# Optimization experiments

Hardware: AMD Instinct MI355X
Metric: run time of the kernel (lower is better)

Reference implementation:

```python
import jax, jax.numpy as jnp
import numpy as np

F, LP, NL, DG = 65536, 8, 8192, 64
D = 32  # path_state_dim == link_state_dim
ITERS = 8
MS = {'flow_traffic': (0.5, 2.0), 'flow_length': (0.5, 2.0), 'flow_loss_packet': (0.1, 5.0),
      'flow_propag_delay': (0.2, 3.0), 'link_capacity': (1.0, 1.0)}


def gru_cell(h, x, w, u, b):
    # Keras GRUCell (reset_after=True); gate order z, r, h
    mx = x @ w + b[0]
    mh = h @ u + b[1]
    xz, xr, xh = jnp.split(mx, 3, axis=-1)
    hz, hr, hh = jnp.split(mh, 3, axis=-1)
    z = jax.nn.sigmoid(xz + hz)
    r = jax.nn.sigmoid(xr + hr)
    c = jnp.tanh(xh + r * hh)
    return z * h + (1.0 - z) * c


def setup_inputs() -> dict:
    key = jax.random.key(0)
    ks = jax.random.split(key, 24)
    g = lambda i, shape: jax.random.normal(ks[i], shape, jnp.float32) * 0.1
    return dict(
        flow_traffic=jax.random.uniform(ks[0], (F, 1), jnp.float32),
        flow_length=jax.random.uniform(ks[1], (F, 1), jnp.float32),
        flow_loss_packet=jax.random.uniform(ks[2], (F, 1), jnp.float32),
        flow_propag_delay=jax.random.uniform(ks[3], (F, 1), jnp.float32),
        flow_packet_size=jax.random.uniform(ks[4], (F, 1), jnp.float32),
        link_capacity=jax.random.uniform(ks[5], (NL, 1), jnp.float32) + 0.5,
        link_to_flow=jax.random.randint(ks[6], (F, LP), 0, NL),
        flow_to_link_flow=jax.random.randint(ks[7], (NL, DG), 0, F),
        flow_to_link_pos=jax.random.randint(ks[8], (NL, DG), 0, LP + 1),
        fe_w1=g(9, (4, D)), fe_b1=jnp.zeros(D), fe_w2=g(10, (D, D)), fe_b2=jnp.zeros(D),
        le_w1=g(11, (2, D)), le_b1=jnp.zeros(D), le_w2=g(12, (D, D)), le_b2=jnp.zeros(D),
        att_w=g(13, (D, D)), att_b=jnp.zeros(D),
        pg_w=g(14, (D, 3 * D)), pg_u=g(15, (D, 3 * D)), pg_b=jnp.zeros((2, 3 * D)),
        lg_w=g(16, (D, 3 * D)), lg_u=g(17, (D, 3 * D)), lg_b=jnp.zeros((2, 3 * D)),
        ro_w1=g(18, (D, D // 2)), ro_b1=jnp.zeros(D // 2),
        ro_w2=g(19, (D // 2, D // 4)), ro_b2=jnp.zeros(D // 4),
        ro_w3=g(20, (D // 4, 1)), ro_b3=jnp.zeros(1),
    )


def reference(flow_traffic, flow_length, flow_loss_packet, flow_propag_delay, flow_packet_size,
              link_capacity, link_to_flow, flow_to_link_flow, flow_to_link_pos,
              fe_w1, fe_b1, fe_w2, fe_b2, le_w1, le_b1, le_w2, le_b2, att_w, att_b,
              pg_w, pg_u, pg_b, lg_w, lg_u, lg_b, ro_w1, ro_b1, ro_w2, ro_b2, ro_w3, ro_b3):
    norm = lambda x, k: (x - MS[k][0]) * MS[k][1]
    # per-link load: mean of traffic of flows crossing it / capacity  -> [NL,1]
    load = jnp.mean(flow_traffic[flow_to_link_flow], axis=1) / link_capacity
    pf = jnp.concatenate([norm(flow_traffic, 'flow_traffic'), norm(flow_length, 'flow_length'),
                          norm(flow_loss_packet, 'flow_loss_packet'),
                          norm(flow_propag_delay, 'flow_propag_delay')], axis=1)
    path_state = jax.nn.selu(jax.nn.selu(pf @ fe_w1 + fe_b1) @ fe_w2 + fe_b2)  # [F,D]
    lf = jnp.concatenate([norm(link_capacity, 'link_capacity'), load], axis=1)
    link_state = jax.nn.selu(jax.nn.selu(lf @ le_w1 + le_b1) @ le_w2 + le_b2)  # [NL,D]

    pss = None
    for _ in range(ITERS):
        link_gather = link_state[link_to_flow]  # [F,LP,D]
        prev = path_state

        def step(h, x):
            h2 = gru_cell(h, x, pg_w, pg_u, pg_b)
            return h2, h2

        path_state, seq = jax.lax.scan(step, prev, jnp.swapaxes(link_gather, 0, 1))
        seq = jnp.swapaxes(seq, 0, 1)  # [F,LP,D]
        pss = jnp.concatenate([prev[:, None, :], seq], axis=1)  # [F,LP+1,D]
        path_gather = pss[flow_to_link_flow, flow_to_link_pos]  # [NL,DG,D]
        attn = jax.nn.leaky_relu(path_gather @ att_w + att_b, negative_slope=0.2)
        score = jax.nn.softmax(attn, axis=-1)  # K.softmax default axis=-1
        agg = jnp.sum(score * path_gather, axis=1)  # [NL,D]
        link_state = gru_cell(link_state, agg, lg_w, lg_u, lg_b)

    h = jax.nn.selu(pss[:, 1:] @ ro_w1 + ro_b1)
    h = jax.nn.selu(h @ ro_w2 + ro_b2)
    occupancy = jax.nn.softplus(h @ ro_w3 + ro_b3)  # [F,LP,1]
    capacity_gather = link_capacity[link_to_flow]  # [F,LP,1]
    delay = jnp.sum(occupancy / capacity_gather, axis=1)  # [F,1]
    return delay + flow_propag_delay
```

## Files before the change

kernel.cpp:

```cpp
#include <hip/hip_runtime.h>
#include <hip/hip_bf16.h>
#include <cstddef>

#define F_    65536
#define LP_   8
#define NL_   8192
#define DG_   64
#define D_    32
#define ITERS_ 8

typedef short bf16x8 __attribute__((ext_vector_type(8)));
typedef float f32x2 __attribute__((ext_vector_type(2)));
typedef float f32x4 __attribute__((ext_vector_type(4)));
typedef float f32x16 __attribute__((ext_vector_type(16)));
typedef unsigned int u32x4 __attribute__((ext_vector_type(4)));


__device__ __forceinline__ float sigmoidf_(float x) { return 1.0f / (1.0f + __expf(-x)); }
__device__ __forceinline__ float tanhf_(float x)    { return 1.0f - 2.0f / (__expf(2.0f * x) + 1.0f); }
__device__ __forceinline__ float seluf_(float x) {
    const float a = 1.6732632423543772f, s = 1.0507009873554805f;
    return x > 0.0f ? s * x : s * a * (__expf(x) - 1.0f);
}
__device__ __forceinline__ float softplusf_(float x) { return x > 20.0f ? x : log1pf(__expf(x)); }

#define REP32(M) M(0)M(1)M(2)M(3)M(4)M(5)M(6)M(7)M(8)M(9)M(10)M(11)M(12)M(13)M(14)M(15) \
                 M(16)M(17)M(18)M(19)M(20)M(21)M(22)M(23)M(24)M(25)M(26)M(27)M(28)M(29)M(30)M(31)

#define BC32(src, i) __int_as_float(__builtin_amdgcn_ds_swizzle(__float_as_int(src), ((i) << 5)))

__device__ __forceinline__ unsigned int cvtpk_bf16(float a, float b) {
    unsigned int r;
    asm("v_cvt_pk_bf16_f32 %0, %1, %2" : "=v"(r) : "v"(a), "v"(b));
    return r;
}
__device__ __forceinline__ float bf_lo(unsigned int u) { return __uint_as_float(u << 16); }
__device__ __forceinline__ float bf_hi(unsigned int u) { return __uint_as_float(u & 0xFFFF0000u); }

__device__ __forceinline__ void mk_frag_w(f32x4 v0, f32x4 v1, u32x4& uh, u32x4& ul) {
    uh.x = cvtpk_bf16(v0.x, v0.y);
    uh.y = cvtpk_bf16(v0.z, v0.w);
    uh.z = cvtpk_bf16(v1.x, v1.y);
    uh.w = cvtpk_bf16(v1.z, v1.w);
    ul.x = cvtpk_bf16(v0.x - bf_lo(uh.x), v0.y - bf_hi(uh.x));
    ul.y = cvtpk_bf16(v0.z - bf_lo(uh.y), v0.w - bf_hi(uh.y));
    ul.z = cvtpk_bf16(v1.x - bf_lo(uh.z), v1.y - bf_hi(uh.z));
    ul.w = cvtpk_bf16(v1.z - bf_lo(uh.w), v1.w - bf_hi(uh.w));
}
__device__ __forceinline__ void mk_frag(f32x4 v0, f32x4 v1, bf16x8& hi, bf16x8& lo) {
    u32x4 uh, ul;
    mk_frag_w(v0, v1, uh, ul);
    hi = __builtin_bit_cast(bf16x8, uh);
    lo = __builtin_bit_cast(bf16x8, ul);
}

__global__ __launch_bounds__(64) void k_prep(
    const float* __restrict__ pg_u, const float* __restrict__ pg_w,
    unsigned int* __restrict__ wpre)
{
    const int lane = threadIdx.x & 63;
    const int jj = lane & 15;
    const int g  = lane >> 4;
    u32x4* wp = (u32x4*)wpre;
    for (int tl = 0; tl < 12; tl++) {
        float v[8];
        if (tl < 6) {
#pragma unroll
            for (int e = 0; e < 8; e++) {
                const int d = 4 * g + (e >> 1) + 16 * (e & 1);
                v[e] = pg_u[d * 96 + tl * 16 + jj];
            }
            u32x4 uh, ul;
            mk_frag_w(f32x4{v[0], v[1], v[2], v[3]}, f32x4{v[4], v[5], v[6], v[7]}, uh, ul);
            wp[tl * 64 + lane] = uh;
            wp[(12 + tl) * 64 + lane] = ul;
        } else {
#pragma unroll
            for (int e = 0; e < 8; e++)
                v[e] = pg_w[(8 * g + e) * 96 + (tl - 6) * 16 + jj];
            u32x4 uh;
            uh.x = cvtpk_bf16(v[0], v[1]);
            uh.y = cvtpk_bf16(v[2], v[3]);
            uh.z = cvtpk_bf16(v[4], v[5]);
            uh.w = cvtpk_bf16(v[6], v[7]);
            wp[tl * 64 + lane] = uh;
        }
    }
}

__global__ __launch_bounds__(256) void k_init_path(
    const float* __restrict__ tr, const float* __restrict__ len,
    const float* __restrict__ loss, const float* __restrict__ prop,
    const float* __restrict__ fe_w1, const float* __restrict__ fe_b1,
    const float* __restrict__ fe_w2, const float* __restrict__ fe_b2,
    float* __restrict__ h32)
{
    const int j = threadIdx.x & 31;
    const int half = (threadIdx.x >> 5) & 1;
    float w2c[32];
#pragma unroll
    for (int i = 0; i < 32; i++) w2c[i] = fe_w2[i * 32 + j];
    const float w10 = fe_w1[j], w11 = fe_w1[32 + j], w12 = fe_w1[64 + j], w13 = fe_w1[96 + j];
    const float b1 = fe_b1[j], b2 = fe_b2[j];
    const int pj = 8 * ((j >> 2) & 3) + 2 * (j & 3) + (j >> 4);
    const int wave = (blockIdx.x * blockDim.x + threadIdx.x) >> 6;
    const int nw = (gridDim.x * blockDim.x) >> 6;
    for (int fp = wave; fp < F_ / 2; fp += nw) {
        const int f = fp * 2 + half;
        float p0 = (tr[f]   - 0.5f) * 2.0f;
        float p1 = (len[f]  - 0.5f) * 2.0f;
        float p2 = (loss[f] - 0.1f) * 5.0f;
        float p3 = (prop[f] - 0.2f) * 3.0f;
        float h1 = seluf_(fmaf(p0, w10, fmaf(p1, w11, fmaf(p2, w12, fmaf(p3, w13, b1)))));
        float acc = b2;
#define ISTEP(i) { float hv = BC32(h1, i); acc = fmaf(hv, w2c[i], acc); }
        REP32(ISTEP)
#undef ISTEP
        h32[(size_t)f * 32 + pj] = seluf_(acc);
    }
}

__global__ __launch_bounds__(256) void k_init_link(
    const float* __restrict__ tr, const float* __restrict__ cap, const int* __restrict__ f2lf,
    const float* __restrict__ le_w1, const float* __restrict__ le_b1,
    const float* __restrict__ le_w2, const float* __restrict__ le_b2,
    float* __restrict__ link_state, unsigned int* __restrict__ ls_pack)
{
    const int lane = threadIdx.x & 63;
    const int j = lane & 31;
    float w2c[32];
#pragma unroll
    for (int i = 0; i < 32; i++) w2c[i] = le_w2[i * 32 + j];
    const float w10 = le_w1[j], w11 = le_w1[32 + j];
    const float b1 = le_b1[j], b2 = le_b2[j];
    const int wave = (blockIdx.x * blockDim.x + threadIdx.x) >> 6;
    const int nw = (gridDim.x * blockDim.x) >> 6;
    for (int l = wave; l < NL_; l += nw) {
        int fidx = f2lf[l * 64 + lane];
        float s = tr[fidx];
        s += __shfl_xor(s, 1);  s += __shfl_xor(s, 2);  s += __shfl_xor(s, 4);
        s += __shfl_xor(s, 8);  s += __shfl_xor(s, 16); s += __shfl_xor(s, 32);
        float c = cap[l];
        float load = s * (1.0f / 64.0f) / c;
        float lf0 = (c - 1.0f);
        float h1 = seluf_(fmaf(lf0, w10, fmaf(load, w11, b1)));
        float acc = b2;
#define LSTEP(i) { float hv = BC32(h1, i); acc = fmaf(hv, w2c[i], acc); }
        REP32(LSTEP)
#undef LSTEP
        float lsv = seluf_(acc);
        float a = __shfl(lsv, 2 * (j & 15));
        float b = __shfl(lsv, 2 * (j & 15) + 1);
        unsigned int hw = cvtpk_bf16(a, b);
        unsigned int lw = cvtpk_bf16(a - bf_lo(hw), b - bf_hi(hw));
        if (lane < 32) {
            link_state[l * 32 + j] = lsv;
            ls_pack[l * 32 + j] = (j < 16) ? hw : lw;
        }
    }
}

__global__ __launch_bounds__(256, 3) void k_path(
    const unsigned int* __restrict__ ls_pack, const unsigned int* __restrict__ wpre,
    const float* __restrict__ pg_b, const int* __restrict__ l2f,
    unsigned short* __restrict__ pss_bf, float* __restrict__ h32)
{
    const int lane = threadIdx.x & 63;
    const int jj   = lane & 15;
    const int g    = lane >> 4;
    const int task = (blockIdx.x * blockDim.x + threadIdx.x) >> 6;
    const int fme  = task * 16 + jj;

    const u32x4* wp = (const u32x4*)wpre;
    u32x4 whi[12], wlo[6];
#pragma unroll
    for (int tl = 0; tl < 12; tl++) whi[tl] = wp[tl * 64 + lane];
#pragma unroll
    for (int tl = 0; tl < 6; tl++)  wlo[tl] = wp[(12 + tl) * 64 + lane];

    float b_z[4][2], b_r[4][2], b0h[4][2], b1h[4][2];
#pragma unroll
    for (int r = 0; r < 4; r++)
#pragma unroll
        for (int hf = 0; hf < 2; hf++) {
            const int d = 16 * hf + 4 * g + r;
            b_z[r][hf] = pg_b[d]      + pg_b[96 + d];
            b_r[r][hf] = pg_b[32 + d] + pg_b[96 + 32 + d];
            b0h[r][hf] = pg_b[64 + d];
            b1h[r][hf] = pg_b[96 + 64 + d];
        }

    unsigned short* pbase = pss_bf + (size_t)fme * 288;
    float* hbase = h32 + (size_t)fme * 32;
    f32x4 v0 = *(const f32x4*)(hbase + 8 * g);
    f32x4 v1 = *(const f32x4*)(hbase + 8 * g + 4);
    u32x4 bhw, blw;
    mk_frag_w(v0, v1, bhw, blw);
    *(u32x4*)(pbase + 8 * g) = bhw;
    float hC[4][2] = {{v0.x, v0.y}, {v0.z, v0.w}, {v1.x, v1.y}, {v1.z, v1.w}};

    const int* lrow = l2f + fme * 8;
    const u32x4* lsp = (const u32x4*)ls_pack;
    u32x4 lsh_n = lsp[lrow[0] * 8 + g];
    unsigned short* pst = pbase + 32 + 8 * g;

#pragma unroll 1
    for (int t = 0; t < 8; ++t) {
        bf16x8 xhi = __builtin_bit_cast(bf16x8, lsh_n);
        int lk_nxt = lrow[(t < 7) ? t + 1 : 7];
        u32x4 ls_pref = lsp[lk_nxt * 8 + g];
        bf16x8 hhi = __builtin_bit_cast(bf16x8, bhw);
        bf16x8 hlo = __builtin_bit_cast(bf16x8, blw);
        f32x4 acc[8];
#pragma unroll
        for (int a = 0; a < 8; a++) acc[a] = f32x4{0.0f, 0.0f, 0.0f, 0.0f};
#pragma unroll
        for (int tl = 0; tl < 6; tl++) {
            bf16x8 ah = __builtin_bit_cast(bf16x8, whi[tl]);
            bf16x8 al = __builtin_bit_cast(bf16x8, wlo[tl]);
            const int a = (tl < 4) ? tl : 4 + (tl & 1);
            acc[a] = __builtin_amdgcn_mfma_f32_16x16x32_bf16(ah, hhi, acc[a], 0, 0, 0);
            acc[a] = __builtin_amdgcn_mfma_f32_16x16x32_bf16(al, hhi, acc[a], 0, 0, 0);
            acc[a] = __builtin_amdgcn_mfma_f32_16x16x32_bf16(ah, hlo, acc[a], 0, 0, 0);
        }
#pragma unroll
        for (int tl = 0; tl < 6; tl++) {
            bf16x8 ah = __builtin_bit_cast(bf16x8, whi[6 + tl]);
            const int a = (tl < 4) ? tl : 6 + (tl & 1);
            acc[a] = __builtin_amdgcn_mfma_f32_16x16x32_bf16(ah, xhi, acc[a], 0, 0, 0);
        }
#pragma unroll
        for (int r = 0; r < 4; r++)
#pragma unroll
            for (int hf = 0; hf < 2; hf++) {
                float z  = sigmoidf_(acc[0 + hf][r] + b_z[r][hf]);
                float rg = sigmoidf_(acc[2 + hf][r] + b_r[r][hf]);
                float c  = tanhf_(acc[6 + hf][r] + b0h[r][hf] + rg * (acc[4 + hf][r] + b1h[r][hf]));
                hC[r][hf] = fmaf(z, hC[r][hf] - c, c);
            }
        bhw.x = cvtpk_bf16(hC[0][0], hC[0][1]);
        bhw.y = cvtpk_bf16(hC[1][0], hC[1][1]);
        bhw.z = cvtpk_bf16(hC[2][0], hC[2][1]);
        bhw.w = cvtpk_bf16(hC[3][0], hC[3][1]);
        blw.x = cvtpk_bf16(hC[0][0] - bf_lo(bhw.x), hC[0][1] - bf_hi(bhw.x));
        blw.y = cvtpk_bf16(hC[1][0] - bf_lo(bhw.y), hC[1][1] - bf_hi(bhw.y));
        blw.z = cvtpk_bf16(hC[2][0] - bf_lo(bhw.z), hC[2][1] - bf_hi(bhw.z));
        blw.w = cvtpk_bf16(hC[3][0] - bf_lo(bhw.w), hC[3][1] - bf_hi(bhw.w));
        *(u32x4*)pst = bhw;
        pst += 32;
        lsh_n = ls_pref;
    }
    *(f32x4*)(hbase + 8 * g)     = f32x4{hC[0][0], hC[0][1], hC[1][0], hC[1][1]};
    *(f32x4*)(hbase + 8 * g + 4) = f32x4{hC[2][0], hC[2][1], hC[3][0], hC[3][1]};
}

__global__ __launch_bounds__(256, 3) void k_att_fused(
    const unsigned short* __restrict__ pss_bf, const int* __restrict__ f2lf, const int* __restrict__ f2lp,
    const float* __restrict__ att_w, const float* __restrict__ att_b,
    const float* __restrict__ lg_w, const float* __restrict__ lg_u, const float* __restrict__ lg_b,
    float* __restrict__ link_state, unsigned int* __restrict__ ls_pack)
{
    __shared__ float xbuf[4][32];
    const int w = threadIdx.x >> 6;
    const int lane = threadIdx.x & 63;
    const int p31 = lane & 31;
    const int h = lane >> 5;
    const int l = blockIdx.x * 4 + w;
    const int j = p31;

    const int fi = f2lf[l * 64 + lane];
    const int pi = f2lp[l * 64 + lane];
    const unsigned int* rowp = (const unsigned int*)(pss_bf + ((size_t)fi * 9 + pi) * 32);
    u32x4 g0 = *(const u32x4*)(rowp + 0);
    u32x4 g1 = *(const u32x4*)(rowp + 4);
    u32x4 g2 = *(const u32x4*)(rowp + 8);
    u32x4 g3 = *(const u32x4*)(rowp + 12);
    unsigned int own[16] = {g0.x, g0.y, g0.z, g0.w, g1.x, g1.y, g1.z, g1.w,
                            g2.x, g2.y, g2.z, g2.w, g3.x, g3.y, g3.z, g3.w};
    unsigned int swp[16];
#pragma unroll
    for (int i = 0; i < 16; i++) swp[i] = __shfl_xor(own[i], 32);

    bf16x8 awhi[2], awlo[2];
#pragma unroll
    for (int kt = 0; kt < 2; kt++) {
        const int B4 = 4 * (2 * kt + h);
        f32x4 a0 = f32x4{att_w[(B4 + 0) * 32 + p31], att_w[(B4 + 16) * 32 + p31],
                         att_w[(B4 + 1) * 32 + p31], att_w[(B4 + 17) * 32 + p31]};
        f32x4 a1 = f32x4{att_w[(B4 + 2) * 32 + p31], att_w[(B4 + 18) * 32 + p31],
                         att_w[(B4 + 3) * 32 + p31], att_w[(B4 + 19) * 32 + p31]};
        mk_frag(a0, a1, awhi[kt], awlo[kt]);
    }
    f32x4 ab[4];
#pragma unroll
    for (int rg = 0; rg < 4; rg++) {
        const float* bp = att_b + 8 * rg + 4 * h;
        ab[rg] = f32x4{bp[0], bp[1], bp[2], bp[3]};
    }

    bf16x8 B0[2], B1[2];
#pragma unroll
    for (int kt = 0; kt < 2; kt++) {
        u32x4 b0, b1;
#pragma unroll
        for (int e = 0; e < 4; e++) {
            unsigned int v0 = h ? swp[8 * kt + 4 + e] : own[8 * kt + e];
            unsigned int v1 = h ? own[8 * kt + 4 + e] : swp[8 * kt + e];
            ((unsigned int*)&b0)[e] = v0;
            ((unsigned int*)&b1)[e] = v1;
        }
        B0[kt] = __builtin_bit_cast(bf16x8, b0);
        B1[kt] = __builtin_bit_cast(bf16x8, b1);
    }

    f32x16 acc0{}, acc1{};
#pragma unroll
    for (int kt = 0; kt < 2; kt++) {
        acc0 = __builtin_amdgcn_mfma_f32_32x32x16_bf16(awhi[kt], B0[kt], acc0, 0, 0, 0);
        acc0 = __builtin_amdgcn_mfma_f32_32x32x16_bf16(awlo[kt], B0[kt], acc0, 0, 0, 0);
        acc1 = __builtin_amdgcn_mfma_f32_32x32x16_bf16(awhi[kt], B1[kt], acc1, 0, 0, 0);
        acc1 = __builtin_amdgcn_mfma_f32_32x32x16_bf16(awlo[kt], B1[kt], acc1, 0, 0, 0);
    }

    float q0[16], q1[16];
#pragma unroll
    for (int ph = 0; ph < 2; ph++) {
        float v[16];
#pragma unroll
        for (int r = 0; r < 16; r++) {
            float bias = ((const float*)&ab[r >> 2])[r & 3];
            float x = (ph == 0 ? acc0[r] : acc1[r]) + bias;
            v[r] = x > 0.0f ? x : 0.2f * x;
        }
        float m = v[0];
#pragma unroll
        for (int r = 1; r < 16; r++) m = fmaxf(m, v[r]);
        m = fmaxf(m, __shfl_xor(m, 32));
        float sm = 0.0f;
#pragma unroll
        for (int r = 0; r < 16; r++) { v[r] = __expf(v[r] - m); sm += v[r]; }
        sm += __shfl_xor(sm, 32);
        float inv = 1.0f / sm;
        float* q = (ph == 0) ? q0 : q1;
#pragma unroll
        for (int r = 0; r < 16; r++) {
            const int q4 = r >> 2, rl = r & 3;
            const int wA = 8 * (q4 & 1) + rl;
            const int wB = 8 * (q4 & 1) + 4 + rl;
            unsigned int pv;
            if (ph == 0) pv = h ? swp[wB] : own[wA];
            else         pv = h ? own[wB] : swp[wA];
            float pf = (q4 & 2) ? bf_hi(pv) : bf_lo(pv);
            q[r] = v[r] * inv * pf;
        }
    }
    float qs[16];
#pragma unroll
    for (int r = 0; r < 16; r++) qs[r] = q0[r] + q1[r];
#pragma unroll
    for (int d = 1; d < 32; d <<= 1) {
#pragma unroll
        for (int r = 0; r < 16; r++) qs[r] += __shfl_xor(qs[r], d);
    }
    if (p31 == 0) {
#pragma unroll
        for (int r = 0; r < 16; r++) xbuf[w][(r & 3) + 8 * (r >> 2) + 4 * h] = qs[r];
    }
    float s = xbuf[w][j];

    const float hval = link_state[l * 32 + j];
    float src = (lane < 32) ? hval : s;
    const float* wb = (lane < 32) ? lg_u : lg_w;
    float p0 = (lane < 32) ? lg_b[96 + j]      : lg_b[j];
    float p1 = (lane < 32) ? lg_b[96 + 32 + j] : lg_b[32 + j];
    float p2 = (lane < 32) ? lg_b[96 + 64 + j] : lg_b[64 + j];
#define ASTEP(i) { float vv = BC32(src, i); \
    p0 = fmaf(vv, wb[(i) * 96 + j], p0); \
    p1 = fmaf(vv, wb[(i) * 96 + 32 + j], p1); \
    p2 = fmaf(vv, wb[(i) * 96 + 64 + j], p2); }
    REP32(ASTEP)
#undef ASTEP
    float t0 = __shfl_xor(p0, 32);
    float t1 = __shfl_xor(p1, 32);
    float t2 = __shfl_xor(p2, 32);
    float hn = 0.0f;
    if (lane < 32) {
        float z = sigmoidf_(t0 + p0);
        float r = sigmoidf_(t1 + p1);
        float c = tanhf_(t2 + r * p2);
        hn = fmaf(z, hval, (1.0f - z) * c);
        link_state[l * 32 + j] = hn;
    }
    float a = __shfl(hn, 2 * (j & 15));
    float b = __shfl(hn, 2 * (j & 15) + 1);
    unsigned int hw = cvtpk_bf16(a, b);
    unsigned int lw = cvtpk_bf16(a - bf_lo(hw), b - bf_hi(hw));
    if (lane < 32) ls_pack[l * 32 + j] = (j < 16) ? hw : lw;
}

__global__ __launch_bounds__(256) void k_readout(
    const unsigned short* __restrict__ pss_bf, const int* __restrict__ l2f,
    const float* __restrict__ cap, const float* __restrict__ prop,
    const float* __restrict__ ro_w1, const float* __restrict__ b1,
    const float* __restrict__ ro_w2, const float* __restrict__ b2,
    const float* __restrict__ w3, const float* __restrict__ b3,
    float* __restrict__ out)
{
    const int tid = blockIdx.x * blockDim.x + threadIdx.x;
    const int f = tid >> 3, t = tid & 7;
    const unsigned int* rowp = (const unsigned int*)(pss_bf + ((size_t)f * 9 + 1 + t) * 32);
    float xr[32];
#pragma unroll
    for (int i = 0; i < 4; i++) {
        u32x4 v = *(const u32x4*)(rowp + 4 * i);
        xr[8 * i + 0] = bf_lo(v.x); xr[8 * i + 1] = bf_hi(v.x);
        xr[8 * i + 2] = bf_lo(v.y); xr[8 * i + 3] = bf_hi(v.y);
        xr[8 * i + 4] = bf_lo(v.z); xr[8 * i + 5] = bf_hi(v.z);
        xr[8 * i + 6] = bf_lo(v.w); xr[8 * i + 7] = bf_hi(v.w);
    }
    float h1[16];
#pragma unroll
    for (int jj = 0; jj < 16; jj++) {
        float acc = b1[jj];
#pragma unroll
        for (int p = 0; p < 32; p++) {
            const int d = 4 * (p >> 3) + ((p & 7) >> 1) + 16 * (p & 1);
            acc = fmaf(xr[p], ro_w1[d * 16 + jj], acc);
        }
        h1[jj] = seluf_(acc);
    }
    float h2[8];
#pragma unroll
    for (int jj = 0; jj < 8; jj++) {
        float acc = b2[jj];
#pragma unroll
        for (int i = 0; i < 16; i++) acc = fmaf(h1[i], ro_w2[i * 8 + jj], acc);
        h2[jj] = seluf_(acc);
    }
    float o = b3[0];
#pragma unroll
    for (int i = 0; i < 8; i++) o = fmaf(h2[i], w3[i], o);
    o = softplusf_(o);
    int link = l2f[f * 8 + t];
    float v = o / cap[link];
    v += __shfl_xor(v, 1, 8);
    v += __shfl_xor(v, 2, 8);
    v += __shfl_xor(v, 4, 8);
    if (t == 0) out[f] = v + prop[f];
}

extern "C" void kernel_launch(void* const* d_in, const int* in_sizes, int n_in,
                              void* d_out, int out_size, void* d_ws, size_t ws_size,
                              hipStream_t stream) {
    const float* flow_traffic = (const float*)d_in[0];
    const float* flow_length  = (const float*)d_in[1];
    const float* flow_loss    = (const float*)d_in[2];
    const float* flow_prop    = (const float*)d_in[3];
    const float* link_cap     = (const float*)d_in[5];
    const int*   l2f          = (const int*)d_in[6];
    const int*   f2lf         = (const int*)d_in[7];
    const int*   f2lp         = (const int*)d_in[8];
    const float* fe_w1 = (const float*)d_in[9],  *fe_b1 = (const float*)d_in[10];
    const float* fe_w2 = (const float*)d_in[11], *fe_b2 = (const float*)d_in[12];
    const float* le_w1 = (const float*)d_in[13], *le_b1 = (const float*)d_in[14];
    const float* le_w2 = (const float*)d_in[15], *le_b2 = (const float*)d_in[16];
    const float* att_w = (const float*)d_in[17], *att_b = (const float*)d_in[18];
    const float* pg_w  = (const float*)d_in[19], *pg_u  = (const float*)d_in[20], *pg_b = (const float*)d_in[21];
    const float* lg_w  = (const float*)d_in[22], *lg_u  = (const float*)d_in[23], *lg_b = (const float*)d_in[24];
    const float* ro_w1 = (const float*)d_in[25], *ro_b1 = (const float*)d_in[26];
    const float* ro_w2 = (const float*)d_in[27], *ro_b2 = (const float*)d_in[28];
    const float* ro_w3 = (const float*)d_in[29], *ro_b3 = (const float*)d_in[30];
    float* out = (float*)d_out;

    unsigned short* pss_bf = (unsigned short*)d_ws;
    float* h32        = (float*)(pss_bf + (size_t)F_ * 288);
    float* link_state = h32 + (size_t)F_ * 32;
    unsigned int* ls_pack = (unsigned int*)(link_state + NL_ * 32);
    unsigned int* wpre    = ls_pack + (size_t)NL_ * 32;

    k_prep<<<1, 64, 0, stream>>>(pg_u, pg_w, wpre);
    k_init_path<<<512, 256, 0, stream>>>(flow_traffic, flow_length, flow_loss, flow_prop,
                                         fe_w1, fe_b1, fe_w2, fe_b2, h32);
    k_init_link<<<512, 256, 0, stream>>>(flow_traffic, link_cap, f2lf,
                                         le_w1, le_b1, le_w2, le_b2, link_state, ls_pack);
    for (int it = 0; it < ITERS_; ++it) {
        k_path<<<F_ / 64, 256, 0, stream>>>(ls_pack, wpre, pg_b, l2f, pss_bf, h32);
        k_att_fused<<<NL_ / 4, 256, 0, stream>>>(pss_bf, f2lf, f2lp, att_w, att_b,
                                                 lg_w, lg_u, lg_b, link_state, ls_pack);
    }
    k_readout<<<F_ * 8 / 256, 256, 0, stream>>>(pss_bf, l2f, link_cap, flow_prop,
                                                ro_w1, ro_b1, ro_w2, ro_b2, ro_w3, ro_b3, out);
}
```

Before: 527.4 us.

## Compute link GRU matmuls with MFMA using pre-packed bf16 weights

Replaces the scalar per-lane FMA loop for the link GRU update in k_att_fused with bf16 MFMA 16x16x32 instructions. The k_prep kernel now also packs lg_w and lg_u into MFMA fragment layout, with a hi/lo split for the recurrent weights and state. The goal is to cut the 96 serial FMAs per lane and the broadcast shuffles in the GRU tail. In exchange the input projection runs in bf16, adding rounding error, and output writes are concentrated in a few lanes.

```diff
diff --git a/kernel.cpp b/kernel.cpp
--- a/kernel.cpp
+++ b/kernel.cpp
@@ -56,6 +56,7 @@
 
 __global__ __launch_bounds__(64) void k_prep(
     const float* __restrict__ pg_u, const float* __restrict__ pg_w,
+    const float* __restrict__ lg_w, const float* __restrict__ lg_u,
     unsigned int* __restrict__ wpre)
 {
     const int lane = threadIdx.x & 63;
@@ -85,6 +86,25 @@
             uh.w = cvtpk_bf16(v[6], v[7]);
             wp[tl * 64 + lane] = uh;
         }
+    }
+    u32x4* wq = wp + 18 * 64;
+    for (int tl = 0; tl < 6; tl++) {
+        float vx[8], vh[8];
+#pragma unroll
+        for (int e = 0; e < 8; e++) {
+            vx[e] = lg_w[(8 * g + e) * 96 + tl * 16 + jj];
+            vh[e] = lg_u[(8 * g + e) * 96 + tl * 16 + jj];
+        }
+        u32x4 xh;
+        xh.x = cvtpk_bf16(vx[0], vx[1]);
+        xh.y = cvtpk_bf16(vx[2], vx[3]);
+        xh.z = cvtpk_bf16(vx[4], vx[5]);
+        xh.w = cvtpk_bf16(vx[6], vx[7]);
+        wq[tl * 64 + lane] = xh;
+        u32x4 uh, ul;
+        mk_frag_w(f32x4{vh[0], vh[1], vh[2], vh[3]}, f32x4{vh[4], vh[5], vh[6], vh[7]}, uh, ul);
+        wq[(6 + tl) * 64 + lane] = uh;
+        wq[(12 + tl) * 64 + lane] = ul;
     }
 }
 
@@ -257,16 +277,17 @@
 __global__ __launch_bounds__(256, 3) void k_att_fused(
     const unsigned short* __restrict__ pss_bf, const int* __restrict__ f2lf, const int* __restrict__ f2lp,
     const float* __restrict__ att_w, const float* __restrict__ att_b,
-    const float* __restrict__ lg_w, const float* __restrict__ lg_u, const float* __restrict__ lg_b,
+    const unsigned int* __restrict__ wgru, const float* __restrict__ lg_b,
     float* __restrict__ link_state, unsigned int* __restrict__ ls_pack)
 {
-    __shared__ float xbuf[4][32];
+    __shared__ __align__(16) float xbuf[4][32];
     const int w = threadIdx.x >> 6;
     const int lane = threadIdx.x & 63;
     const int p31 = lane & 31;
     const int h = lane >> 5;
     const int l = blockIdx.x * 4 + w;
-    const int j = p31;
+    const int jq = lane & 15;
+    const int gq = lane >> 4;
 
     const int fi = f2lf[l * 64 + lane];
     const int pi = f2lp[l * 64 + lane];
@@ -366,36 +387,78 @@
 #pragma unroll
         for (int r = 0; r < 16; r++) xbuf[w][(r & 3) + 8 * (r >> 2) + 4 * h] = qs[r];
     }
-    float s = xbuf[w][j];
-
-    const float hval = link_state[l * 32 + j];
-    float src = (lane < 32) ? hval : s;
-    const float* wb = (lane < 32) ? lg_u : lg_w;
-    float p0 = (lane < 32) ? lg_b[96 + j]      : lg_b[j];
-    float p1 = (lane < 32) ? lg_b[96 + 32 + j] : lg_b[32 + j];
-    float p2 = (lane < 32) ? lg_b[96 + 64 + j] : lg_b[64 + j];
-#define ASTEP(i) { float vv = BC32(src, i); \
-    p0 = fmaf(vv, wb[(i) * 96 + j], p0); \
-    p1 = fmaf(vv, wb[(i) * 96 + 32 + j], p1); \
-    p2 = fmaf(vv, wb[(i) * 96 + 64 + j], p2); }
-    REP32(ASTEP)
-#undef ASTEP
-    float t0 = __shfl_xor(p0, 32);
-    float t1 = __shfl_xor(p1, 32);
-    float t2 = __shfl_xor(p2, 32);
-    float hn = 0.0f;
-    if (lane < 32) {
-        float z = sigmoidf_(t0 + p0);
-        float r = sigmoidf_(t1 + p1);
-        float c = tanhf_(t2 + r * p2);
-        hn = fmaf(z, hval, (1.0f - z) * c);
-        link_state[l * 32 + j] = hn;
-    }
-    float a = __shfl(hn, 2 * (j & 15));
-    float b = __shfl(hn, 2 * (j & 15) + 1);
-    unsigned int hw = cvtpk_bf16(a, b);
-    unsigned int lw = cvtpk_bf16(a - bf_lo(hw), b - bf_hi(hw));
-    if (lane < 32) ls_pack[l * 32 + j] = (j < 16) ? hw : lw;
+
+    f32x4 xa = *(const f32x4*)&xbuf[w][8 * gq];
+    f32x4 xb = *(const f32x4*)&xbuf[w][8 * gq + 4];
+    u32x4 xw;
+    xw.x = cvtpk_bf16(xa.x, xa.y); xw.y = cvtpk_bf16(xa.z, xa.w);
+    xw.z = cvtpk_bf16(xb.x, xb.y); xw.w = cvtpk_bf16(xb.z, xb.w);
+    bf16x8 Bx = __builtin_bit_cast(bf16x8, xw);
+    const float* lrow = link_state + l * 32;
+    f32x4 ha = *(const f32x4*)(lrow + 8 * gq);
+    f32x4 hb = *(const f32x4*)(lrow + 8 * gq + 4);
+    u32x4 hw_, hlw_;
+    mk_frag_w(ha, hb, hw_, hlw_);
+    bf16x8 Bh  = __builtin_bit_cast(bf16x8, hw_);
+    bf16x8 Bhl = __builtin_bit_cast(bf16x8, hlw_);
+    float hv[4][2];
+#pragma unroll
+    for (int r = 0; r < 4; r++)
+#pragma unroll
+        for (int hf = 0; hf < 2; hf++)
+            hv[r][hf] = lrow[16 * hf + 4 * gq + r];
+
+    const u32x4* wq = (const u32x4*)wgru;
+    f32x4 gacc[8];
+#pragma unroll
+    for (int a = 0; a < 8; a++) gacc[a] = f32x4{0.0f, 0.0f, 0.0f, 0.0f};
+#pragma unroll
+    for (int tl = 0; tl < 6; tl++) {
+        bf16x8 Ax = __builtin_bit_cast(bf16x8, wq[tl * 64 + lane]);
+        const int a = (tl < 4) ? tl : 6 + (tl & 1);
+        gacc[a] = __builtin_amdgcn_mfma_f32_16x16x32_bf16(Ax, Bx, gacc[a], 0, 0, 0);
+    }
+#pragma unroll
+    for (int tl = 0; tl < 6; tl++) {
+        bf16x8 Ah = __builtin_bit_cast(bf16x8, wq[(6 + tl) * 64 + lane]);
+        bf16x8 Al = __builtin_bit_cast(bf16x8, wq[(12 + tl) * 64 + lane]);
+        const int a = (tl < 4) ? tl : 4 + (tl & 1);
+        gacc[a] = __builtin_amdgcn_mfma_f32_16x16x32_bf16(Ah, Bh, gacc[a], 0, 0, 0);
+        gacc[a] = __builtin_amdgcn_mfma_f32_16x16x32_bf16(Al, Bh, gacc[a], 0, 0, 0);
+        gacc[a] = __builtin_amdgcn_mfma_f32_16x16x32_bf16(Ah, Bhl, gacc[a], 0, 0, 0);
+    }
+    float hn[4][2];
+#pragma unroll
+    for (int r = 0; r < 4; r++)
+#pragma unroll
+        for (int hf = 0; hf < 2; hf++) {
+            const int d = 16 * hf + 4 * gq + r;
+            float z  = sigmoidf_(gacc[0 + hf][r] + lg_b[d] + lg_b[96 + d]);
+            float rg = sigmoidf_(gacc[2 + hf][r] + lg_b[32 + d] + lg_b[96 + 32 + d]);
+            float c  = tanhf_(gacc[6 + hf][r] + lg_b[64 + d] + rg * (gacc[4 + hf][r] + lg_b[96 + 64 + d]));
+            hn[r][hf] = fmaf(z, hv[r][hf] - c, c);
+        }
+    if (jq == 0) {
+        float* lsw = link_state + l * 32;
+#pragma unroll
+        for (int r = 0; r < 4; r++) {
+            lsw[4 * gq + r]      = hn[r][0];
+            lsw[16 + 4 * gq + r] = hn[r][1];
+        }
+        unsigned int* pk = ls_pack + l * 32;
+        unsigned int w0 = cvtpk_bf16(hn[0][0], hn[1][0]);
+        unsigned int w1 = cvtpk_bf16(hn[2][0], hn[3][0]);
+        unsigned int w2 = cvtpk_bf16(hn[0][1], hn[1][1]);
+        unsigned int w3w = cvtpk_bf16(hn[2][1], hn[3][1]);
+        pk[2 * gq]         = w0;
+        pk[2 * gq + 1]     = w1;
+        pk[8 + 2 * gq]     = w2;
+        pk[8 + 2 * gq + 1] = w3w;
+        pk[16 + 2 * gq]         = cvtpk_bf16(hn[0][0] - bf_lo(w0), hn[1][0] - bf_hi(w0));
+        pk[16 + 2 * gq + 1]     = cvtpk_bf16(hn[2][0] - bf_lo(w1), hn[3][0] - bf_hi(w1));
+        pk[16 + 8 + 2 * gq]     = cvtpk_bf16(hn[0][1] - bf_lo(w2), hn[1][1] - bf_hi(w2));
+        pk[16 + 8 + 2 * gq + 1] = cvtpk_bf16(hn[2][1] - bf_lo(w3w), hn[3][1] - bf_hi(w3w));
+    }
 }
 
 __global__ __launch_bounds__(256) void k_readout(
@@ -477,8 +540,9 @@
     float* link_state = h32 + (size_t)F_ * 32;
     unsigned int* ls_pack = (unsigned int*)(link_state + NL_ * 32);
     unsigned int* wpre    = ls_pack + (size_t)NL_ * 32;
-
-    k_prep<<<1, 64, 0, stream>>>(pg_u, pg_w, wpre);
+    unsigned int* wgru    = wpre + 18 * 64 * 4;
+
+    k_prep<<<1, 64, 0, stream>>>(pg_u, pg_w, lg_w, lg_u, wpre);
     k_init_path<<<512, 256, 0, stream>>>(flow_traffic, flow_length, flow_loss, flow_prop,
                                          fe_w1, fe_b1, fe_w2, fe_b2, h32);
     k_init_link<<<512, 256, 0, stream>>>(flow_traffic, link_cap, f2lf,
@@ -486,7 +550,7 @@
     for (int it = 0; it < ITERS_; ++it) {
         k_path<<<F_ / 64, 256, 0, stream>>>(ls_pack, wpre, pg_b, l2f, pss_bf, h32);
         k_att_fused<<<NL_ / 4, 256, 0, stream>>>(pss_bf, f2lf, f2lp, att_w, att_b,
-                                                 lg_w, lg_u, lg_b, link_state, ls_pack);
+                                                 wgru, lg_b, link_state, ls_pack);
     }
     k_readout<<<F_ * 8 / 256, 256, 0, stream>>>(pss_bf, l2f, link_cap, flow_prop,
                                                 ro_w1, ro_b1, ro_w2, ro_b2, ro_w3, ro_b3, out);
```

Result: slower. 582.5 us (+10.4%).
